# Optimization experiments

Hardware: AMD Instinct MI355X
Metric: run time of the kernel (lower is better)

## Reference

```python
import jax, jax.numpy as jnp
import numpy as np

N = 50000
E = 800000
IN_DIM = 128
HID = 64
OUT_DIM = 1
NEG_SLOPE = 0.2
EPS = 1e-16


def _glorot(key, shape):
    fan = shape[-1] + (shape[0] if len(shape) > 1 else shape[-1])
    lim = jnp.sqrt(6.0 / fan)
    return jax.random.uniform(key, shape, jnp.float32, -lim, lim)


def setup_inputs() -> dict:
    key = jax.random.key(0)
    ks = jax.random.split(key, 12)
    x = jax.random.normal(ks[0], (N, IN_DIM), jnp.float32)
    edge_index = jax.random.randint(ks[1], (2, E), 0, N, jnp.int64)
    # GATConv layer 1: in=128, out=64, heads=4, concat=True
    W1 = _glorot(ks[2], (4 * HID, IN_DIM))
    att_src1 = _glorot(ks[3], (4, HID))
    att_dst1 = _glorot(ks[4], (4, HID))
    b1 = jnp.zeros((4 * HID,), jnp.float32)
    # GATConv layer 2: in=256, out=64, heads=1, concat=True
    W2 = _glorot(ks[5], (HID, 4 * HID))
    att_src2 = _glorot(ks[6], (1, HID))
    att_dst2 = _glorot(ks[7], (1, HID))
    b2 = jnp.zeros((HID,), jnp.float32)
    # final Linear(hidden, 1)
    fc_w = _glorot(ks[8], (OUT_DIM, HID))
    fc_b = jnp.zeros((OUT_DIM,), jnp.float32)
    return {"x": x, "edge_index": edge_index, "W1": W1, "att_src1": att_src1,
            "att_dst1": att_dst1, "b1": b1, "W2": W2, "att_src2": att_src2,
            "att_dst2": att_dst2, "b2": b2, "fc_w": fc_w, "fc_b": fc_b}


def _gat_layer(x, src, dst, W, att_src, att_dst, bias, heads, out_ch):
    n = x.shape[0]
    xt = (x @ W.T).reshape(n, heads, out_ch)          # [N, H, C]
    a_src = jnp.sum(xt * att_src[None], axis=-1)      # [N, H]
    a_dst = jnp.sum(xt * att_dst[None], axis=-1)      # [N, H]
    e = a_src[src] + a_dst[dst]                       # [E', H]
    e = jnp.where(e > 0, e, NEG_SLOPE * e)            # LeakyReLU(0.2)
    # segment softmax over incoming edges of each dst node
    m = jax.ops.segment_max(e, dst, num_segments=n)
    e = jnp.exp(e - m[dst])
    s = jax.ops.segment_sum(e, dst, num_segments=n)
    alpha = e / (s[dst] + EPS)                        # [E', H]
    msg = xt[src] * alpha[:, :, None]                 # [E', H, C]
    out = jax.ops.segment_sum(msg, dst, num_segments=n)
    return out.reshape(n, heads * out_ch) + bias


def reference(x, edge_index, W1, att_src1, att_dst1, b1,
              W2, att_src2, att_dst2, b2, fc_w, fc_b):
    n = x.shape[0]
    # PyG GATConv default: add self-loops
    loops = jnp.arange(n, dtype=edge_index.dtype)
    src = jnp.concatenate([edge_index[0], loops])
    dst = jnp.concatenate([edge_index[1], loops])
    h = jax.nn.relu(_gat_layer(x, src, dst, W1, att_src1, att_dst1, b1, 4, HID))
    h = jax.nn.relu(_gat_layer(h, src, dst, W2, att_src2, att_dst2, b2, 1, HID))
    logits = h @ fc_w.T + fc_b                        # [N, 1]
    return jax.nn.sigmoid(logits).squeeze()
```

## Files before the change

### kernel.cpp

```cpp
#include <hip/hip_runtime.h>
#include <hip/hip_bf16.h>

#define NN 50000
#define EE 800000
#define ET (NN + EE)
#define SG ((NN + 255) / 256)
#define GB1 ((NN + 63) / 64)

typedef __attribute__((ext_vector_type(8))) short short8;
typedef __attribute__((ext_vector_type(4))) short short4b;
typedef __attribute__((ext_vector_type(4))) float f32x4;

__device__ __forceinline__ float bf2f(unsigned short u) {
    union { unsigned int i; float f; } v; v.i = ((unsigned int)u) << 16; return v.f;
}
__device__ __forceinline__ unsigned short f2bf(float f) {
    __hip_bfloat16 h = __float2bfloat16(f);
    return *reinterpret_cast<unsigned short*>(&h);
}
__device__ __forceinline__ float lrelu(float e) { return fmaxf(e, 0.2f * e); }


__global__ void k_hist(const int* __restrict__ dst, int* __restrict__ cnt,
                       const float* __restrict__ W1, unsigned short* __restrict__ w1b,
                       const float* __restrict__ W2, unsigned short* __restrict__ w2b) {
    int t = threadIdx.x;
    int b = blockIdx.x;
    if (b < 32) {
        int j = b * 256 + t;
        float4 v = *(const float4*)(W1 + j * 4);
        short4b o;
        o[0] = (short)f2bf(v.x); o[1] = (short)f2bf(v.y);
        o[2] = (short)f2bf(v.z); o[3] = (short)f2bf(v.w);
        *(short4b*)(w1b + j * 4) = o;
    } else if (b < 48) {
        int j = (b - 32) * 256 + t;
        float4 v = *(const float4*)(W2 + j * 4);
        short4b o;
        o[0] = (short)f2bf(v.x); o[1] = (short)f2bf(v.y);
        o[2] = (short)f2bf(v.z); o[3] = (short)f2bf(v.w);
        *(short4b*)(w2b + j * 4) = o;
    }
    int i = b * blockDim.x + t;
    if (i < EE) atomicAdd(&cnt[dst[i]], 1);
}

__global__ __launch_bounds__(256) void k_scan1(const int* __restrict__ cnt,
                                               int* __restrict__ tmp, int* __restrict__ bsum) {
    int b = blockIdx.x, t = threadIdx.x, i = b * 256 + t;
    int lane = t & 63, w = t >> 6;
    int v = (i < NN) ? cnt[i] : 0;
    int s = v;
    #pragma unroll
    for (int off = 1; off < 64; off <<= 1) {
        int u = __shfl_up(s, off);
        if (lane >= off) s += u;
    }
    __shared__ int ws[4];
    if (lane == 63) ws[w] = s;
    __syncthreads();
    if (t == 0) {
        int a = 0;
        #pragma unroll
        for (int k = 0; k < 4; k++) { int x = ws[k]; ws[k] = a; a += x; }
        bsum[b] = a;
    }
    __syncthreads();
    s += ws[w];
    if (i < NN) tmp[i] = s;
}

__global__ __launch_bounds__(256) void k_scan2(const int* __restrict__ bsum, int* __restrict__ boff) {
    int t = threadIdx.x, lane = t & 63, w = t >> 6;
    int v = (t < SG) ? bsum[t] : 0;
    int s = v;
    #pragma unroll
    for (int off = 1; off < 64; off <<= 1) {
        int u = __shfl_up(s, off);
        if (lane >= off) s += u;
    }
    __shared__ int ws[4];
    if (lane == 63) ws[w] = s;
    __syncthreads();
    if (t == 0) {
        int a = 0;
        #pragma unroll
        for (int k = 0; k < 4; k++) { int x = ws[k]; ws[k] = a; a += x; }
    }
    __syncthreads();
    s += ws[w];
    if (t < SG) boff[t] = s - v;
}

__global__ void k_scan3_prep(const int* __restrict__ tmp, const int* __restrict__ boff,
                             int* __restrict__ rowptr, int* __restrict__ writeptr,
                             int* __restrict__ csr) {
    int i = blockIdx.x * blockDim.x + threadIdx.x;
    if (i == 0) rowptr[0] = 0;
    if (i < NN) {
        int base = boff[i >> 8];
        int incl = tmp[i] + base + i + 1;
        rowptr[i + 1] = incl;
        int excl = ((i & 255) ? tmp[i - 1] + base : base) + i;
        csr[excl] = i;
        writeptr[i] = excl + 1;
    }
}

template<int K, int N, int NH, bool A_BF16, bool B_BF16>
__device__ __forceinline__ void gemm_body(
    int bid, const void* __restrict__ Aptr, const void* __restrict__ Wptr,
    const float* __restrict__ atts, const float* __restrict__ attd,
    unsigned short* __restrict__ C, float* __restrict__ as_, float* __restrict__ ad_,
    int M)
{
    constexpr int KU  = K / 8;
    constexpr int KUH = KU / 2;
    constexpr int KC  = K / 32;
    constexpr int NW  = N / 4;
    constexpr int NI  = NW / 16;
    constexpr int ABYTES = 64 * KU * 16;
    constexpr int BBYTES = N * KUH * 16;
    constexpr int SMEM = ABYTES + BBYTES + (NH == 1 ? 2048 : 0);
    __shared__ char smem[SMEM];
    char* Ash = smem;
    char* Bsh = smem + ABYTES;
    unsigned short* Csh = (unsigned short*)smem;
    float* scsh = (float*)(smem + ABYTES + BBYTES);

    int t = threadIdx.x;
    int lane = t & 63, w = t >> 6;
    int colL = lane & 15, quad = lane >> 4;
    int m0 = bid * 64;

    {
        constexpr int CNT = 64 * KU / 256;
        #pragma unroll
        for (int i = 0; i < CNT; i++) {
            int v = t + 256 * i;
            int m = v / KU, u = v % KU;
            int gr = m0 + m; if (gr >= M) gr = M - 1;
            short8 val;
            if (A_BF16) {
                val = *(const short8*)((const unsigned short*)Aptr + (size_t)gr * K + u * 8);
            } else {
                const float* Af = (const float*)Aptr;
                float4 lo = *(const float4*)(Af + (size_t)gr * K + u * 8);
                float4 hi = *(const float4*)(Af + (size_t)gr * K + u * 8 + 4);
                val[0] = (short)f2bf(lo.x); val[1] = (short)f2bf(lo.y);
                val[2] = (short)f2bf(lo.z); val[3] = (short)f2bf(lo.w);
                val[4] = (short)f2bf(hi.x); val[5] = (short)f2bf(hi.y);
                val[6] = (short)f2bf(hi.z); val[7] = (short)f2bf(hi.w);
            }
            *(short8*)(Ash + ((size_t)m * KU + (u ^ (m & 7))) * 16) = val;
        }
    }

    f32x4 acc[4][NI];
    #pragma unroll
    for (int mi = 0; mi < 4; mi++)
        #pragma unroll
        for (int ni = 0; ni < NI; ni++) acc[mi][ni] = (f32x4){0.f, 0.f, 0.f, 0.f};

    #pragma unroll
    for (int kh = 0; kh < 2; kh++) {
        __syncthreads();
        {
            constexpr int CNT = N * KUH / 256;
            #pragma unroll
            for (int i = 0; i < CNT; i++) {
                int v = t + 256 * i;
                int n = v / KUH, uu = v % KUH;
                int u = kh * KUH + uu;
                short8 val;
                if (B_BF16) {
                    val = *(const short8*)((const unsigned short*)Wptr + (size_t)n * K + u * 8);
                } else {
                    const float* Wf = (const float*)Wptr;
                    float4 lo = *(const float4*)(Wf + (size_t)n * K + u * 8);
                    float4 hi = *(const float4*)(Wf + (size_t)n * K + u * 8 + 4);
                    val[0] = (short)f2bf(lo.x); val[1] = (short)f2bf(lo.y);
                    val[2] = (short)f2bf(lo.z); val[3] = (short)f2bf(lo.w);
                    val[4] = (short)f2bf(hi.x); val[5] = (short)f2bf(hi.y);
                    val[6] = (short)f2bf(hi.z); val[7] = (short)f2bf(hi.w);
                }
                *(short8*)(Bsh + ((size_t)n * KUH + (uu ^ (n & 7))) * 16) = val;
            }
        }
        __syncthreads();
        #pragma unroll
        for (int kcl = 0; kcl < KC / 2; kcl++) {
            int uA = (kh * (KC / 2) + kcl) * 4 + quad;
            int uB = kcl * 4 + quad;
            short8 bfr[NI];
            #pragma unroll
            for (int ni = 0; ni < NI; ni++) {
                int n = w * NW + ni * 16 + colL;
                bfr[ni] = *(const short8*)(Bsh + ((size_t)n * KUH + (uB ^ (n & 7))) * 16);
            }
            #pragma unroll
            for (int mi = 0; mi < 4; mi++) {
                int m = mi * 16 + colL;
                short8 af = *(const short8*)(Ash + ((size_t)m * KU + (uA ^ (m & 7))) * 16);
                #pragma unroll
                for (int ni = 0; ni < NI; ni++)
                    acc[mi][ni] = __builtin_amdgcn_mfma_f32_16x16x32_bf16(af, bfr[ni], acc[mi][ni], 0, 0, 0);
            }
        }
    }
    __syncthreads();

    float asv[NI], adv[NI];
    #pragma unroll
    for (int ni = 0; ni < NI; ni++) {
        int na = (NH == 4) ? (w * 64 + ni * 16 + colL) : (w * 16 + colL);
        asv[ni] = atts[na];
        adv[ni] = attd[na];
    }
    #pragma unroll
    for (int mi = 0; mi < 4; mi++) {
        float ps[4] = {0.f, 0.f, 0.f, 0.f}, pd[4] = {0.f, 0.f, 0.f, 0.f};
        #pragma unroll
        for (int ni = 0; ni < NI; ni++)
            #pragma unroll
            for (int r = 0; r < 4; r++) {
                ps[r] += acc[mi][ni][r] * asv[ni];
                pd[r] += acc[mi][ni][r] * adv[ni];
            }
        #pragma unroll
        for (int off = 1; off < 16; off <<= 1)
            #pragma unroll
            for (int r = 0; r < 4; r++) {
                ps[r] += __shfl_xor(ps[r], off);
                pd[r] += __shfl_xor(pd[r], off);
            }
        if (colL == 0) {
            #pragma unroll
            for (int r = 0; r < 4; r++) {
                int rloc = mi * 16 + quad * 4 + r;
                if (NH == 4) {
                    int row = m0 + rloc;
                    if (row < M) {
                        as_[(size_t)row * 4 + w] = ps[r];
                        ad_[(size_t)row * 4 + w] = pd[r];
                    }
                } else {
                    scsh[(w * 64 + rloc) * 2 + 0] = ps[r];
                    scsh[(w * 64 + rloc) * 2 + 1] = pd[r];
                }
            }
        }
    }

    #pragma unroll
    for (int mi = 0; mi < 4; mi++)
        #pragma unroll
        for (int ni = 0; ni < NI; ni++)
            #pragma unroll
            for (int r = 0; r < 4; r++)
                Csh[(size_t)(mi * 16 + quad * 4 + r) * (N + 8) + w * NW + ni * 16 + colL] =
                    f2bf(acc[mi][ni][r]);
    __syncthreads();

    {
        constexpr int CNT = 64 * (N / 8) / 256;
        #pragma unroll
        for (int i = 0; i < CNT; i++) {
            int v = t + 256 * i;
            int m = v / (N / 8), u = v % (N / 8);
            int row = m0 + m;
            if (row < M)
                *(short8*)(C + (size_t)row * N + u * 8) =
                    *(const short8*)(Csh + (size_t)m * (N + 8) + u * 8);
        }
    }
    if (NH == 1 && t < 64) {
        int row = m0 + t;
        if (row < M) {
            float s = 0.f, d = 0.f;
            #pragma unroll
            for (int ww = 0; ww < 4; ww++) {
                s += scsh[(ww * 64 + t) * 2 + 0];
                d += scsh[(ww * 64 + t) * 2 + 1];
            }
            as_[row] = s;
            ad_[row] = d;
        }
    }
}

template<int K, int N, int NH, bool A_BF16, bool B_BF16>
__global__ __launch_bounds__(256) void k_gemm_mfma(
    const void* __restrict__ Aptr, const void* __restrict__ Wptr,
    const float* __restrict__ atts, const float* __restrict__ attd,
    unsigned short* __restrict__ C, float* __restrict__ as_, float* __restrict__ ad_,
    int M)
{
    gemm_body<K, N, NH, A_BF16, B_BF16>(blockIdx.x, Aptr, Wptr, atts, attd, C, as_, ad_, M);
}

__global__ __launch_bounds__(256) void k_gemm1_scatter(
    const void* __restrict__ Aptr, const void* __restrict__ Wptr,
    const float* __restrict__ atts, const float* __restrict__ attd,
    unsigned short* __restrict__ C, float* __restrict__ as_, float* __restrict__ ad_,
    int M,
    const int* __restrict__ src, const int* __restrict__ dst,
    int* __restrict__ writeptr, int* __restrict__ csr)
{
    int bid = blockIdx.x;
    int g = bid / 5, r = bid % 5;
    if (r == 0 && g < GB1) {
        gemm_body<128, 256, 4, false, true>(g, Aptr, Wptr, atts, attd, C, as_, ad_, M);
    } else {
        int ng = (r == 0) ? g : g + 1;
        if (ng > GB1) ng = GB1;
        int sb = bid - ng;
        int i = sb * 256 + threadIdx.x;
        if (i < EE) {
            int pos = atomicAdd(&writeptr[dst[i]], 1);
            csr[pos] = src[i];
        }
    }
}

__global__ __launch_bounds__(256) void k_l1_agg(
    const unsigned short* __restrict__ xt1, const float* __restrict__ as1,
    const float* __restrict__ ad1, const int* __restrict__ rowptr,
    const int* __restrict__ csr, const float* __restrict__ b1,
    unsigned short* __restrict__ h1)
{
    int t = threadIdx.x;
    int lane = t & 63, w = t >> 6;
    int n = blockIdx.x * 4 + w;
    int beg = rowptr[n], deg = rowptr[n + 1] - beg;
    int half = lane >> 5, c = lane & 31, h = c >> 3;
    float adh = ad1[n * 4 + h];
    const char* xb = (const char*)xt1;
    const char* ab = (const char*)as1;
    unsigned co = (unsigned)(c << 4);
    unsigned ho = (unsigned)(h << 2);

    float acc[8] = {0.f, 0.f, 0.f, 0.f, 0.f, 0.f, 0.f, 0.f};
    float esum = 0.f;
    int j = 0;
    for (; j + 8 <= deg; j += 8) {
        int p = beg + j + half * 4;
        int s0 = csr[p], s1 = csr[p + 1], s2 = csr[p + 2], s3 = csr[p + 3];
        float a0 = *(const float*)(ab + ((unsigned)(s0 << 4) + ho));
        float a1 = *(const float*)(ab + ((unsigned)(s1 << 4) + ho));
        float a2 = *(const float*)(ab + ((unsigned)(s2 << 4) + ho));
        float a3 = *(const float*)(ab + ((unsigned)(s3 << 4) + ho));
        short8 r0 = *(const short8*)(xb + ((unsigned)(s0 << 9) + co));
        short8 r1 = *(const short8*)(xb + ((unsigned)(s1 << 9) + co));
        short8 r2 = *(const short8*)(xb + ((unsigned)(s2 << 9) + co));
        short8 r3 = *(const short8*)(xb + ((unsigned)(s3 << 9) + co));
        float e0 = __expf(lrelu(a0 + adh));
        float e1 = __expf(lrelu(a1 + adh));
        float e2 = __expf(lrelu(a2 + adh));
        float e3 = __expf(lrelu(a3 + adh));
        esum += (e0 + e1) + (e2 + e3);
        #pragma unroll
        for (int k = 0; k < 8; k++)
            acc[k] += (bf2f((unsigned short)r0[k]) * e0 + bf2f((unsigned short)r1[k]) * e1)
                    + (bf2f((unsigned short)r2[k]) * e2 + bf2f((unsigned short)r3[k]) * e3);
    }
    if (j + 4 <= deg) {
        int p = beg + j + half * 2;
        int s0 = csr[p], s1 = csr[p + 1];
        float a0 = *(const float*)(ab + ((unsigned)(s0 << 4) + ho));
        float a1 = *(const float*)(ab + ((unsigned)(s1 << 4) + ho));
        short8 r0 = *(const short8*)(xb + ((unsigned)(s0 << 9) + co));
        short8 r1 = *(const short8*)(xb + ((unsigned)(s1 << 9) + co));
        float e0 = __expf(lrelu(a0 + adh));
        float e1 = __expf(lrelu(a1 + adh));
        esum += e0 + e1;
        #pragma unroll
        for (int k = 0; k < 8; k++)
            acc[k] += bf2f((unsigned short)r0[k]) * e0 + bf2f((unsigned short)r1[k]) * e1;
        j += 4;
    }
    for (; j < deg; j += 2) {
        int jj = j + half;
        if (jj < deg) {
            int s = csr[beg + jj];
            float a0 = *(const float*)(ab + ((unsigned)(s << 4) + ho));
            short8 r = *(const short8*)(xb + ((unsigned)(s << 9) + co));
            float e = __expf(lrelu(a0 + adh));
            esum += e;
            #pragma unroll
            for (int k = 0; k < 8; k++) acc[k] += bf2f((unsigned short)r[k]) * e;
        }
    }
    #pragma unroll
    for (int k = 0; k < 8; k++) acc[k] += __shfl_xor(acc[k], 32);
    esum += __shfl_xor(esum, 32);
    if (half == 0) {
        float rs = 1.f / (esum + 1e-16f);
        float4 bl = *(const float4*)(b1 + c * 8);
        float4 bh = *(const float4*)(b1 + c * 8 + 4);
        float bb[8] = {bl.x, bl.y, bl.z, bl.w, bh.x, bh.y, bh.z, bh.w};
        short8 o;
        #pragma unroll
        for (int k = 0; k < 8; k++)
            o[k] = (short)f2bf(fmaxf(acc[k] * rs + bb[k], 0.f));
        *(short8*)(h1 + (size_t)n * 256 + c * 8) = o;
    }
}

__global__ __launch_bounds__(256) void k_l2_agg(
    const unsigned short* __restrict__ xt2, const float* __restrict__ as2,
    const float* __restrict__ ad2, const int* __restrict__ rowptr,
    const int* __restrict__ csr, const float* __restrict__ b2,
    const float* __restrict__ fcw, const float* __restrict__ fcb,
    float* __restrict__ out)
{
    int t = threadIdx.x;
    int lane = t & 63, w = t >> 6;
    int n = blockIdx.x * 4 + w;
    int beg = rowptr[n], deg = rowptr[n + 1] - beg;
    int q = lane >> 4, c = lane & 15;
    float adv = ad2[n];
    const char* xb = (const char*)xt2;
    unsigned co = (unsigned)(c << 3);

    float acc[4] = {0.f, 0.f, 0.f, 0.f};
    float esum = 0.f;
    int j = 0;
    if (deg >= 16) {
        int p = beg + q * 4;
        int s0 = csr[p], s1 = csr[p + 1], s2 = csr[p + 2], s3 = csr[p + 3];
        float a0 = as2[s0], a1 = as2[s1], a2 = as2[s2], a3 = as2[s3];
        uint2 r0 = *(const uint2*)(xb + ((unsigned)(s0 << 7) + co));
        uint2 r1 = *(const uint2*)(xb + ((unsigned)(s1 << 7) + co));
        uint2 r2 = *(const uint2*)(xb + ((unsigned)(s2 << 7) + co));
        uint2 r3 = *(const uint2*)(xb + ((unsigned)(s3 << 7) + co));
        for (; j + 32 <= deg; j += 16) {
            int p2 = beg + j + 16 + q * 4;
            int u0 = csr[p2], u1 = csr[p2 + 1], u2 = csr[p2 + 2], u3 = csr[p2 + 3];
            float f0 = as2[u0], f1 = as2[u1], f2 = as2[u2], f3 = as2[u3];
            uint2 q0 = *(const uint2*)(xb + ((unsigned)(u0 << 7) + co));
            uint2 q1 = *(const uint2*)(xb + ((unsigned)(u1 << 7) + co));
            uint2 q2 = *(const uint2*)(xb + ((unsigned)(u2 << 7) + co));
            uint2 q3 = *(const uint2*)(xb + ((unsigned)(u3 << 7) + co));
            float e0 = __expf(lrelu(a0 + adv));
            float e1 = __expf(lrelu(a1 + adv));
            float e2 = __expf(lrelu(a2 + adv));
            float e3 = __expf(lrelu(a3 + adv));
            esum += (e0 + e1) + (e2 + e3);
            acc[0] += (bf2f((unsigned short)(r0.x & 0xffff)) * e0 + bf2f((unsigned short)(r1.x & 0xffff)) * e1)
                    + (bf2f((unsigned short)(r2.x & 0xffff)) * e2 + bf2f((unsigned short)(r3.x & 0xffff)) * e3);
            acc[1] += (bf2f((unsigned short)(r0.x >> 16)) * e0 + bf2f((unsigned short)(r1.x >> 16)) * e1)
                    + (bf2f((unsigned short)(r2.x >> 16)) * e2 + bf2f((unsigned short)(r3.x >> 16)) * e3);
            acc[2] += (bf2f((unsigned short)(r0.y & 0xffff)) * e0 + bf2f((unsigned short)(r1.y & 0xffff)) * e1)
                    + (bf2f((unsigned short)(r2.y & 0xffff)) * e2 + bf2f((unsigned short)(r3.y & 0xffff)) * e3);
            acc[3] += (bf2f((unsigned short)(r0.y >> 16)) * e0 + bf2f((unsigned short)(r1.y >> 16)) * e1)
                    + (bf2f((unsigned short)(r2.y >> 16)) * e2 + bf2f((unsigned short)(r3.y >> 16)) * e3);
            a0 = f0; a1 = f1; a2 = f2; a3 = f3;
            r0 = q0; r1 = q1; r2 = q2; r3 = q3;
        }
        {
            float e0 = __expf(lrelu(a0 + adv));
            float e1 = __expf(lrelu(a1 + adv));
            float e2 = __expf(lrelu(a2 + adv));
            float e3 = __expf(lrelu(a3 + adv));
            esum += (e0 + e1) + (e2 + e3);
            acc[0] += (bf2f((unsigned short)(r0.x & 0xffff)) * e0 + bf2f((unsigned short)(r1.x & 0xffff)) * e1)
                    + (bf2f((unsigned short)(r2.x & 0xffff)) * e2 + bf2f((unsigned short)(r3.x & 0xffff)) * e3);
            acc[1] += (bf2f((unsigned short)(r0.x >> 16)) * e0 + bf2f((unsigned short)(r1.x >> 16)) * e1)
                    + (bf2f((unsigned short)(r2.x >> 16)) * e2 + bf2f((unsigned short)(r3.x >> 16)) * e3);
            acc[2] += (bf2f((unsigned short)(r0.y & 0xffff)) * e0 + bf2f((unsigned short)(r1.y & 0xffff)) * e1)
                    + (bf2f((unsigned short)(r2.y & 0xffff)) * e2 + bf2f((unsigned short)(r3.y & 0xffff)) * e3);
            acc[3] += (bf2f((unsigned short)(r0.y >> 16)) * e0 + bf2f((unsigned short)(r1.y >> 16)) * e1)
                    + (bf2f((unsigned short)(r2.y >> 16)) * e2 + bf2f((unsigned short)(r3.y >> 16)) * e3);
            j += 16;
        }
    }
    if (j + 8 <= deg) {
        int p = beg + j + q * 2;
        int s0 = csr[p], s1 = csr[p + 1];
        float a0 = as2[s0], a1 = as2[s1];
        uint2 r0 = *(const uint2*)(xb + ((unsigned)(s0 << 7) + co));
        uint2 r1 = *(const uint2*)(xb + ((unsigned)(s1 << 7) + co));
        float e0 = __expf(lrelu(a0 + adv));
        float e1 = __expf(lrelu(a1 + adv));
        esum += e0 + e1;
        acc[0] += bf2f((unsigned short)(r0.x & 0xffff)) * e0 + bf2f((unsigned short)(r1.x & 0xffff)) * e1;
        acc[1] += bf2f((unsigned short)(r0.x >> 16)) * e0 + bf2f((unsigned short)(r1.x >> 16)) * e1;
        acc[2] += bf2f((unsigned short)(r0.y & 0xffff)) * e0 + bf2f((unsigned short)(r1.y & 0xffff)) * e1;
        acc[3] += bf2f((unsigned short)(r0.y >> 16)) * e0 + bf2f((unsigned short)(r1.y >> 16)) * e1;
        j += 8;
    }
    for (; j < deg; j += 4) {
        int jj = j + q;
        if (jj < deg) {
            int s = csr[beg + jj];
            float a0 = as2[s];
            uint2 r = *(const uint2*)(xb + ((unsigned)(s << 7) + co));
            float e = __expf(lrelu(a0 + adv));
            esum += e;
            acc[0] += bf2f((unsigned short)(r.x & 0xffff)) * e;
            acc[1] += bf2f((unsigned short)(r.x >> 16)) * e;
            acc[2] += bf2f((unsigned short)(r.y & 0xffff)) * e;
            acc[3] += bf2f((unsigned short)(r.y >> 16)) * e;
        }
    }
    #pragma unroll
    for (int k = 0; k < 4; k++) {
        acc[k] += __shfl_xor(acc[k], 16);
        acc[k] += __shfl_xor(acc[k], 32);
    }
    esum += __shfl_xor(esum, 16);
    esum += __shfl_xor(esum, 32);
    float rs = 1.f / (esum + 1e-16f);
    float4 bv = *(const float4*)(b2 + c * 4);
    float4 fv = *(const float4*)(fcw + c * 4);
    float z = fmaxf(acc[0] * rs + bv.x, 0.f) * fv.x
            + fmaxf(acc[1] * rs + bv.y, 0.f) * fv.y
            + fmaxf(acc[2] * rs + bv.z, 0.f) * fv.z
            + fmaxf(acc[3] * rs + bv.w, 0.f) * fv.w;
    #pragma unroll
    for (int off = 8; off; off >>= 1) z += __shfl_xor(z, off);
    if (lane == 0) out[n] = 1.f / (1.f + __expf(-(z + fcb[0])));
}


extern "C" void kernel_launch(void* const* d_in, const int* in_sizes, int n_in,
                              void* d_out, int out_size, void* d_ws, size_t ws_size,
                              hipStream_t stream) {
    const float* x    = (const float*)d_in[0];
    const int*   ei   = (const int*)d_in[1];
    const float* W1   = (const float*)d_in[2];
    const float* as1w = (const float*)d_in[3];
    const float* ad1w = (const float*)d_in[4];
    const float* b1   = (const float*)d_in[5];
    const float* W2   = (const float*)d_in[6];
    const float* as2w = (const float*)d_in[7];
    const float* ad2w = (const float*)d_in[8];
    const float* b2   = (const float*)d_in[9];
    const float* fcw  = (const float*)d_in[10];
    const float* fcb  = (const float*)d_in[11];
    float* out = (float*)d_out;

    const int* src = ei;
    const int* dst = ei + EE;

    char* base = (char*)d_ws;
    size_t off = 0;
    auto alloc = [&](size_t bytes) -> void* {
        void* p = base + off;
        off = (off + bytes + 255) & ~(size_t)255;
        return p;
    };
    int*   rowptr   = (int*)alloc((NN + 1) * sizeof(int));
    int*   cnt      = (int*)alloc(NN * sizeof(int));
    int*   tmp      = (int*)alloc(NN * sizeof(int));
    int*   bsum     = (int*)alloc(SG * sizeof(int));
    int*   boff     = (int*)alloc(SG * sizeof(int));
    int*   writeptr = (int*)alloc(NN * sizeof(int));
    int*   csr      = (int*)alloc(ET * sizeof(int));
    unsigned short* xt1 = (unsigned short*)alloc((size_t)NN * 256 * sizeof(unsigned short));
    unsigned short* h1  = (unsigned short*)alloc((size_t)NN * 256 * sizeof(unsigned short));
    unsigned short* w1b = (unsigned short*)alloc(256 * 128 * sizeof(unsigned short));
    unsigned short* w2b = (unsigned short*)alloc(64 * 256 * sizeof(unsigned short));
    float* as1      = (float*)alloc(NN * 4 * sizeof(float));
    float* ad1      = (float*)alloc(NN * 4 * sizeof(float));
    float* as2      = (float*)alloc(NN * sizeof(float));
    float* ad2      = (float*)alloc(NN * sizeof(float));
    unsigned short* xt2 = xt1;

    hipMemsetAsync(cnt, 0, NN * sizeof(int), stream);
    k_hist<<<(EE + 255) / 256, 256, 0, stream>>>(dst, cnt, W1, w1b, W2, w2b);
    k_scan1<<<SG, 256, 0, stream>>>(cnt, tmp, bsum);
    k_scan2<<<1, 256, 0, stream>>>(bsum, boff);
    k_scan3_prep<<<SG, 256, 0, stream>>>(tmp, boff, rowptr, writeptr, csr);

    int fused_blocks = GB1 + (EE + 255) / 256;
    k_gemm1_scatter<<<fused_blocks, 256, 0, stream>>>(
        x, w1b, as1w, ad1w, xt1, as1, ad1, NN, src, dst, writeptr, csr);

    k_l1_agg<<<(NN + 3) / 4, 256, 0, stream>>>(xt1, as1, ad1, rowptr, csr, b1, h1);
    k_gemm_mfma<256, 64, 1, true, true><<<GB1, 256, 0, stream>>>(
        h1, w2b, as2w, ad2w, xt2, as2, ad2, NN);
    k_l2_agg<<<(NN + 3) / 4, 256, 0, stream>>>(xt2, as2, ad2, rowptr, csr, b2, fcw, fcb, out);
}
```

Baseline: 281.8 us.

## Store layer-1 features in 32-channel slices and split aggregation per slice

The layer-1 GEMM output is now written as eight column slices of 32 channels each, every slice stored contiguously across nodes. The aggregation kernel launches eight blocks per node group, one per slice, so each gather reads 64-byte rows from a 3.2 MB slice instead of 512-byte rows from the full matrix. The aim is better L2 locality for the random neighbor gathers. In exchange, the CSR indices and attention scores are re-read eight times, and the exp for each edge is recomputed once per slice (twice per head).

```diff
diff --git a/kernel.cpp b/kernel.cpp
--- a/kernel.cpp
+++ b/kernel.cpp
@@ -107,7 +107,7 @@
     }
 }
 
-template<int K, int N, int NH, bool A_BF16, bool B_BF16>
+template<int K, int N, int NH, bool A_BF16, bool B_BF16, bool C_SLICED>
 __device__ __forceinline__ void gemm_body(
     int bid, const void* __restrict__ Aptr, const void* __restrict__ Wptr,
     const float* __restrict__ atts, const float* __restrict__ attd,
@@ -269,9 +269,15 @@
             int v = t + 256 * i;
             int m = v / (N / 8), u = v % (N / 8);
             int row = m0 + m;
-            if (row < M)
-                *(short8*)(C + (size_t)row * N + u * 8) =
-                    *(const short8*)(Csh + (size_t)m * (N + 8) + u * 8);
+            if (row < M) {
+                short8 val = *(const short8*)(Csh + (size_t)m * (N + 8) + u * 8);
+                if (C_SLICED) {
+                    int sl = u >> 2, inner = u & 3;
+                    *(short8*)(C + (size_t)sl * ((size_t)NN * 32) + (size_t)row * 32 + inner * 8) = val;
+                } else {
+                    *(short8*)(C + (size_t)row * N + u * 8) = val;
+                }
+            }
         }
     }
     if (NH == 1 && t < 64) {
@@ -289,14 +295,14 @@
     }
 }
 
-template<int K, int N, int NH, bool A_BF16, bool B_BF16>
+template<int K, int N, int NH, bool A_BF16, bool B_BF16, bool C_SLICED>
 __global__ __launch_bounds__(256) void k_gemm_mfma(
     const void* __restrict__ Aptr, const void* __restrict__ Wptr,
     const float* __restrict__ atts, const float* __restrict__ attd,
     unsigned short* __restrict__ C, float* __restrict__ as_, float* __restrict__ ad_,
     int M)
 {
-    gemm_body<K, N, NH, A_BF16, B_BF16>(blockIdx.x, Aptr, Wptr, atts, attd, C, as_, ad_, M);
+    gemm_body<K, N, NH, A_BF16, B_BF16, C_SLICED>(blockIdx.x, Aptr, Wptr, atts, attd, C, as_, ad_, M);
 }
 
 __global__ __launch_bounds__(256) void k_gemm1_scatter(
@@ -310,7 +316,7 @@
     int bid = blockIdx.x;
     int g = bid / 5, r = bid % 5;
     if (r == 0 && g < GB1) {
-        gemm_body<128, 256, 4, false, true>(g, Aptr, Wptr, atts, attd, C, as_, ad_, M);
+        gemm_body<128, 256, 4, false, true, true>(g, Aptr, Wptr, atts, attd, C, as_, ad_, M);
     } else {
         int ng = (r == 0) ? g : g + 1;
         if (ng > GB1) ng = GB1;
@@ -324,86 +330,83 @@
 }
 
 __global__ __launch_bounds__(256) void k_l1_agg(
-    const unsigned short* __restrict__ xt1, const float* __restrict__ as1,
+    const unsigned short* __restrict__ xts, const float* __restrict__ as1,
     const float* __restrict__ ad1, const int* __restrict__ rowptr,
     const int* __restrict__ csr, const float* __restrict__ b1,
     unsigned short* __restrict__ h1)
 {
     int t = threadIdx.x;
     int lane = t & 63, w = t >> 6;
-    int n = blockIdx.x * 4 + w;
+    int s = blockIdx.x & 7;
+    int n = (blockIdx.x >> 3) * 4 + w;
+    int h = s >> 1;
+    int q = lane >> 4, c = lane & 15;
     int beg = rowptr[n], deg = rowptr[n + 1] - beg;
-    int half = lane >> 5, c = lane & 31, h = c >> 3;
-    float adh = ad1[n * 4 + h];
-    const char* xb = (const char*)xt1;
+    float adh = ad1[(n << 2) + h];
+    const char* xb = (const char*)xts + (size_t)s * ((size_t)NN * 64);
     const char* ab = (const char*)as1;
-    unsigned co = (unsigned)(c << 4);
+    unsigned co = (unsigned)(c << 2);
     unsigned ho = (unsigned)(h << 2);
 
-    float acc[8] = {0.f, 0.f, 0.f, 0.f, 0.f, 0.f, 0.f, 0.f};
-    float esum = 0.f;
+    float acc0 = 0.f, acc1 = 0.f, esum = 0.f;
     int j = 0;
-    for (; j + 8 <= deg; j += 8) {
-        int p = beg + j + half * 4;
+    for (; j + 16 <= deg; j += 16) {
+        int p = beg + j + q * 4;
         int s0 = csr[p], s1 = csr[p + 1], s2 = csr[p + 2], s3 = csr[p + 3];
         float a0 = *(const float*)(ab + ((unsigned)(s0 << 4) + ho));
         float a1 = *(const float*)(ab + ((unsigned)(s1 << 4) + ho));
         float a2 = *(const float*)(ab + ((unsigned)(s2 << 4) + ho));
         float a3 = *(const float*)(ab + ((unsigned)(s3 << 4) + ho));
-        short8 r0 = *(const short8*)(xb + ((unsigned)(s0 << 9) + co));
-        short8 r1 = *(const short8*)(xb + ((unsigned)(s1 << 9) + co));
-        short8 r2 = *(const short8*)(xb + ((unsigned)(s2 << 9) + co));
-        short8 r3 = *(const short8*)(xb + ((unsigned)(s3 << 9) + co));
+        unsigned r0 = *(const unsigned*)(xb + ((unsigned)(s0 << 6) + co));
+        unsigned r1 = *(const unsigned*)(xb + ((unsigned)(s1 << 6) + co));
+        unsigned r2 = *(const unsigned*)(xb + ((unsigned)(s2 << 6) + co));
+        unsigned r3 = *(const unsigned*)(xb + ((unsigned)(s3 << 6) + co));
         float e0 = __expf(lrelu(a0 + adh));
         float e1 = __expf(lrelu(a1 + adh));
         float e2 = __expf(lrelu(a2 + adh));
         float e3 = __expf(lrelu(a3 + adh));
         esum += (e0 + e1) + (e2 + e3);
-        #pragma unroll
-        for (int k = 0; k < 8; k++)
-            acc[k] += (bf2f((unsigned short)r0[k]) * e0 + bf2f((unsigned short)r1[k]) * e1)
-                    + (bf2f((unsigned short)r2[k]) * e2 + bf2f((unsigned short)r3[k]) * e3);
-    }
-    if (j + 4 <= deg) {
-        int p = beg + j + half * 2;
+        acc0 += (bf2f((unsigned short)(r0 & 0xffff)) * e0 + bf2f((unsigned short)(r1 & 0xffff)) * e1)
+              + (bf2f((unsigned short)(r2 & 0xffff)) * e2 + bf2f((unsigned short)(r3 & 0xffff)) * e3);
+        acc1 += (bf2f((unsigned short)(r0 >> 16)) * e0 + bf2f((unsigned short)(r1 >> 16)) * e1)
+              + (bf2f((unsigned short)(r2 >> 16)) * e2 + bf2f((unsigned short)(r3 >> 16)) * e3);
+    }
+    if (j + 8 <= deg) {
+        int p = beg + j + q * 2;
         int s0 = csr[p], s1 = csr[p + 1];
         float a0 = *(const float*)(ab + ((unsigned)(s0 << 4) + ho));
         float a1 = *(const float*)(ab + ((unsigned)(s1 << 4) + ho));
-        short8 r0 = *(const short8*)(xb + ((unsigned)(s0 << 9) + co));
-        short8 r1 = *(const short8*)(xb + ((unsigned)(s1 << 9) + co));
+        unsigned r0 = *(const unsigned*)(xb + ((unsigned)(s0 << 6) + co));
+        unsigned r1 = *(const unsigned*)(xb + ((unsigned)(s1 << 6) + co));
         float e0 = __expf(lrelu(a0 + adh));
         float e1 = __expf(lrelu(a1 + adh));
         esum += e0 + e1;
-        #pragma unroll
-        for (int k = 0; k < 8; k++)
-            acc[k] += bf2f((unsigned short)r0[k]) * e0 + bf2f((unsigned short)r1[k]) * e1;
-        j += 4;
-    }
-    for (; j < deg; j += 2) {
-        int jj = j + half;
+        acc0 += bf2f((unsigned short)(r0 & 0xffff)) * e0 + bf2f((unsigned short)(r1 & 0xffff)) * e1;
+        acc1 += bf2f((unsigned short)(r0 >> 16)) * e0 + bf2f((unsigned short)(r1 >> 16)) * e1;
+        j += 8;
+    }
+    for (; j < deg; j += 4) {
+        int jj = j + q;
         if (jj < deg) {
-            int s = csr[beg + jj];
-            float a0 = *(const float*)(ab + ((unsigned)(s << 4) + ho));
-            short8 r = *(const short8*)(xb + ((unsigned)(s << 9) + co));
-            float e = __expf(lrelu(a0 + adh));
-            esum += e;
-            #pragma unroll
-            for (int k = 0; k < 8; k++) acc[k] += bf2f((unsigned short)r[k]) * e;
-        }
-    }
-    #pragma unroll
-    for (int k = 0; k < 8; k++) acc[k] += __shfl_xor(acc[k], 32);
-    esum += __shfl_xor(esum, 32);
-    if (half == 0) {
+            int s0 = csr[beg + jj];
+            float a0 = *(const float*)(ab + ((unsigned)(s0 << 4) + ho));
+            unsigned r0 = *(const unsigned*)(xb + ((unsigned)(s0 << 6) + co));
+            float e0 = __expf(lrelu(a0 + adh));
+            esum += e0;
+            acc0 += bf2f((unsigned short)(r0 & 0xffff)) * e0;
+            acc1 += bf2f((unsigned short)(r0 >> 16)) * e0;
+        }
+    }
+    acc0 += __shfl_xor(acc0, 16); acc0 += __shfl_xor(acc0, 32);
+    acc1 += __shfl_xor(acc1, 16); acc1 += __shfl_xor(acc1, 32);
+    esum += __shfl_xor(esum, 16); esum += __shfl_xor(esum, 32);
+    if (q == 0) {
         float rs = 1.f / (esum + 1e-16f);
-        float4 bl = *(const float4*)(b1 + c * 8);
-        float4 bh = *(const float4*)(b1 + c * 8 + 4);
-        float bb[8] = {bl.x, bl.y, bl.z, bl.w, bh.x, bh.y, bh.z, bh.w};
-        short8 o;
-        #pragma unroll
-        for (int k = 0; k < 8; k++)
-            o[k] = (short)f2bf(fmaxf(acc[k] * rs + bb[k], 0.f));
-        *(short8*)(h1 + (size_t)n * 256 + c * 8) = o;
+        int ch = s * 32 + c * 2;
+        float o0 = fmaxf(acc0 * rs + b1[ch], 0.f);
+        float o1 = fmaxf(acc1 * rs + b1[ch + 1], 0.f);
+        unsigned pack = (unsigned)f2bf(o0) | ((unsigned)f2bf(o1) << 16);
+        *(unsigned*)((char*)h1 + (size_t)n * 512 + ch * 2) = pack;
     }
 }
 
@@ -558,7 +561,7 @@
     int*   boff     = (int*)alloc(SG * sizeof(int));
     int*   writeptr = (int*)alloc(NN * sizeof(int));
     int*   csr      = (int*)alloc(ET * sizeof(int));
-    unsigned short* xt1 = (unsigned short*)alloc((size_t)NN * 256 * sizeof(unsigned short));
+    unsigned short* xts = (unsigned short*)alloc((size_t)NN * 256 * sizeof(unsigned short));
     unsigned short* h1  = (unsigned short*)alloc((size_t)NN * 256 * sizeof(unsigned short));
     unsigned short* w1b = (unsigned short*)alloc(256 * 128 * sizeof(unsigned short));
     unsigned short* w2b = (unsigned short*)alloc(64 * 256 * sizeof(unsigned short));
@@ -566,7 +569,7 @@
     float* ad1      = (float*)alloc(NN * 4 * sizeof(float));
     float* as2      = (float*)alloc(NN * sizeof(float));
     float* ad2      = (float*)alloc(NN * sizeof(float));
-    unsigned short* xt2 = xt1;
+    unsigned short* xt2 = xts;
 
     hipMemsetAsync(cnt, 0, NN * sizeof(int), stream);
     k_hist<<<(EE + 255) / 256, 256, 0, stream>>>(dst, cnt, W1, w1b, W2, w2b);
@@ -576,10 +579,11 @@
 
     int fused_blocks = GB1 + (EE + 255) / 256;
     k_gemm1_scatter<<<fused_blocks, 256, 0, stream>>>(
-        x, w1b, as1w, ad1w, xt1, as1, ad1, NN, src, dst, writeptr, csr);
-
-    k_l1_agg<<<(NN + 3) / 4, 256, 0, stream>>>(xt1, as1, ad1, rowptr, csr, b1, h1);
-    k_gemm_mfma<256, 64, 1, true, true><<<GB1, 256, 0, stream>>>(
+        x, w1b, as1w, ad1w, xts, as1, ad1, NN, src, dst, writeptr, csr);
+
+    k_l1_agg<<<(NN / 4) * 8, 256, 0, stream>>>(xts, as1, ad1, rowptr, csr, b1, h1);
+
+    k_gemm_mfma<256, 64, 1, true, true, false><<<GB1, 256, 0, stream>>>(
         h1, w2b, as2w, ad2w, xt2, as2, ad2, NN);
     k_l2_agg<<<(NN + 3) / 4, 256, 0, stream>>>(xt2, as2, ad2, rowptr, csr, b2, fcw, fcb, out);
 }
```

New measurement: 360.5 us. 27.9% more time.

## Build CSR with histogram-captured ranks instead of second atomic scatter pass

Applied to the files above, without the earlier changes.

The histogram kernel now records each edge's atomicAdd return value as its rank within its destination segment. A new scatter kernel writes csr entries directly at rowptr+1+rank with vectorized int4 loads, replacing the atomic writeptr scatter. That scatter was fused with the layer-1 GEMM, and the fusion is undone so the GEMM runs as its own kernel. This removes the second round of contended atomics but adds an E-sized rank buffer write/read and gives up the overlap of the scatter with the GEMM.

```diff
diff --git a/kernel.cpp b/kernel.cpp
--- a/kernel.cpp
+++ b/kernel.cpp
@@ -22,6 +22,7 @@
 
 
 __global__ void k_hist(const int* __restrict__ dst, int* __restrict__ cnt,
+                       int* __restrict__ rank,
                        const float* __restrict__ W1, unsigned short* __restrict__ w1b,
                        const float* __restrict__ W2, unsigned short* __restrict__ w2b) {
     int t = threadIdx.x;
@@ -42,7 +43,7 @@
         *(short4b*)(w2b + j * 4) = o;
     }
     int i = b * blockDim.x + t;
-    if (i < EE) atomicAdd(&cnt[dst[i]], 1);
+    if (i < EE) rank[i] = atomicAdd(&cnt[dst[i]], 1);
 }
 
 __global__ __launch_bounds__(256) void k_scan1(const int* __restrict__ cnt,
@@ -93,8 +94,7 @@
 }
 
 __global__ void k_scan3_prep(const int* __restrict__ tmp, const int* __restrict__ boff,
-                             int* __restrict__ rowptr, int* __restrict__ writeptr,
-                             int* __restrict__ csr) {
+                             int* __restrict__ rowptr, int* __restrict__ csr) {
     int i = blockIdx.x * blockDim.x + threadIdx.x;
     if (i == 0) rowptr[0] = 0;
     if (i < NN) {
@@ -103,7 +103,24 @@
         rowptr[i + 1] = incl;
         int excl = ((i & 255) ? tmp[i - 1] + base : base) + i;
         csr[excl] = i;
-        writeptr[i] = excl + 1;
+    }
+}
+
+__global__ __launch_bounds__(256) void k_scatter(
+    const int* __restrict__ src, const int* __restrict__ dst,
+    const int* __restrict__ rank, const int* __restrict__ rowptr,
+    int* __restrict__ csr)
+{
+    int i4 = blockIdx.x * blockDim.x + threadIdx.x;
+    if (i4 < EE / 4) {
+        int base = i4 * 4;
+        int4 d = *(const int4*)(dst + base);
+        int4 r = *(const int4*)(rank + base);
+        int4 s = *(const int4*)(src + base);
+        csr[rowptr[d.x] + 1 + r.x] = s.x;
+        csr[rowptr[d.y] + 1 + r.y] = s.y;
+        csr[rowptr[d.z] + 1 + r.z] = s.z;
+        csr[rowptr[d.w] + 1 + r.w] = s.w;
     }
 }
 
@@ -297,30 +314,6 @@
     int M)
 {
     gemm_body<K, N, NH, A_BF16, B_BF16>(blockIdx.x, Aptr, Wptr, atts, attd, C, as_, ad_, M);
-}
-
-__global__ __launch_bounds__(256) void k_gemm1_scatter(
-    const void* __restrict__ Aptr, const void* __restrict__ Wptr,
-    const float* __restrict__ atts, const float* __restrict__ attd,
-    unsigned short* __restrict__ C, float* __restrict__ as_, float* __restrict__ ad_,
-    int M,
-    const int* __restrict__ src, const int* __restrict__ dst,
-    int* __restrict__ writeptr, int* __restrict__ csr)
-{
-    int bid = blockIdx.x;
-    int g = bid / 5, r = bid % 5;
-    if (r == 0 && g < GB1) {
-        gemm_body<128, 256, 4, false, true>(g, Aptr, Wptr, atts, attd, C, as_, ad_, M);
-    } else {
-        int ng = (r == 0) ? g : g + 1;
-        if (ng > GB1) ng = GB1;
-        int sb = bid - ng;
-        int i = sb * 256 + threadIdx.x;
-        if (i < EE) {
-            int pos = atomicAdd(&writeptr[dst[i]], 1);
-            csr[pos] = src[i];
-        }
-    }
 }
 
 __global__ __launch_bounds__(256) void k_l1_agg(
@@ -556,7 +549,7 @@
     int*   tmp      = (int*)alloc(NN * sizeof(int));
     int*   bsum     = (int*)alloc(SG * sizeof(int));
     int*   boff     = (int*)alloc(SG * sizeof(int));
-    int*   writeptr = (int*)alloc(NN * sizeof(int));
+    int*   rank     = (int*)alloc(EE * sizeof(int));
     int*   csr      = (int*)alloc(ET * sizeof(int));
     unsigned short* xt1 = (unsigned short*)alloc((size_t)NN * 256 * sizeof(unsigned short));
     unsigned short* h1  = (unsigned short*)alloc((size_t)NN * 256 * sizeof(unsigned short));
@@ -569,14 +562,14 @@
     unsigned short* xt2 = xt1;
 
     hipMemsetAsync(cnt, 0, NN * sizeof(int), stream);
-    k_hist<<<(EE + 255) / 256, 256, 0, stream>>>(dst, cnt, W1, w1b, W2, w2b);
+    k_hist<<<(EE + 255) / 256, 256, 0, stream>>>(dst, cnt, rank, W1, w1b, W2, w2b);
     k_scan1<<<SG, 256, 0, stream>>>(cnt, tmp, bsum);
     k_scan2<<<1, 256, 0, stream>>>(bsum, boff);
-    k_scan3_prep<<<SG, 256, 0, stream>>>(tmp, boff, rowptr, writeptr, csr);
-
-    int fused_blocks = GB1 + (EE + 255) / 256;
-    k_gemm1_scatter<<<fused_blocks, 256, 0, stream>>>(
-        x, w1b, as1w, ad1w, xt1, as1, ad1, NN, src, dst, writeptr, csr);
+    k_scan3_prep<<<SG, 256, 0, stream>>>(tmp, boff, rowptr, csr);
+    k_scatter<<<(EE / 4 + 255) / 256, 256, 0, stream>>>(src, dst, rank, rowptr, csr);
+
+    k_gemm_mfma<128, 256, 4, false, true><<<GB1, 256, 0, stream>>>(
+        x, w1b, as1w, ad1w, xt1, as1, ad1, NN);
 
     k_l1_agg<<<(NN + 3) / 4, 256, 0, stream>>>(xt1, as1, ad1, rowptr, csr, b1, h1);
     k_gemm_mfma<256, 64, 1, true, true><<<GB1, 256, 0, stream>>>(
```

Result: faster. 268.5 us (-4.7%).
